# Kernel optimization log

Measured on AMD Instinct MI355X. Metric: run time of the kernel, lower is better.

Reference implementation:

```python
import jax, jax.numpy as jnp
import numpy as np

SIGMA = 2.0
INF = 1.0e6
M, N, H, K, C_IN, C_OUT = 50000, 100000, 32, 15, 64, 64
RADIUS = 2.5


def setup_inputs() -> dict:
    key = jax.random.key(0)
    k1, k2, k3, k4, k5, k6 = jax.random.split(key, 6)
    q_points = jax.random.normal(k1, (M, 3), dtype=jnp.float32)
    s_points = jax.random.normal(k2, (N, 3), dtype=jnp.float32)
    s_feats = jax.random.normal(k3, (N, C_IN), dtype=jnp.float32)
    # index N refers to the padding point (placed at INF)
    neighbor_indices = jax.random.randint(k4, (M, H), 0, N + 1, dtype=jnp.int64)
    weights = jax.random.normal(k5, (K, C_IN, C_OUT), dtype=jnp.float32) * 0.05
    # kernel points inside sphere of RADIUS (stand-in for load_kernels buffer)
    kp = jax.random.normal(k6, (K, 3), dtype=jnp.float32)
    kp = kp / jnp.linalg.norm(kp, axis=1, keepdims=True) * RADIUS * 0.7
    kernel_points = kp.at[0].set(0.0)  # fixed='center'
    return {
        "q_points": q_points,
        "s_points": s_points,
        "s_feats": s_feats,
        "neighbor_indices": neighbor_indices,
        "weights": weights,
        "kernel_points": kernel_points,
    }


def reference(q_points, s_points, s_feats, neighbor_indices, weights, kernel_points):
    # pad support points with an 'infinity' shadow point at index N
    padded_pts = jnp.concatenate([s_points, jnp.full((1, 3), INF, s_points.dtype)], axis=0)
    neighbors = padded_pts[neighbor_indices]                    # (M, H, 3)
    rel = neighbors - q_points[:, None, :]                      # (M, H, 3)
    diff = rel[:, :, None, :] - kernel_points[None, None]       # (M, H, K, 3)
    sq_dist = jnp.sum(diff * diff, axis=-1)                     # (M, H, K)
    nbr_w = jnp.clip(1.0 - jnp.sqrt(sq_dist) / SIGMA, 0.0)      # (M, H, K)

    padded_feats = jnp.concatenate([s_feats, jnp.zeros((1, s_feats.shape[1]), s_feats.dtype)], axis=0)
    nbr_feats = padded_feats[neighbor_indices]                  # (M, H, C_in)

    weighted = jnp.einsum('mhk,mhc->mkc', nbr_w, nbr_feats)     # (M, K, C_in)
    out = jnp.einsum('mkc,kcd->md', weighted, weights)          # (M, C_out)

    # normalize by count of real (non-padding / nonzero-sum) neighbors
    nbr_sum = jnp.sum(nbr_feats, axis=-1)                       # (M, H)
    nbr_num = jnp.sum(nbr_sum > 0.0, axis=-1)                   # (M,)
    nbr_num = jnp.maximum(nbr_num, 1)
    return out / nbr_num[:, None].astype(out.dtype)
```

## Files before the change

### kernel.cpp

```cpp
#include <hip/hip_runtime.h>
#include <hip/hip_bf16.h>

#define MPTS 50000
#define NPTS 100000
#define KK 15
#define TM 16
#define NTILES (MPTS / TM)
#define PGRID 512
#define WTP 1028
#define STP 36
#define STPH 20

typedef __attribute__((ext_vector_type(8))) short short8;
typedef __attribute__((ext_vector_type(4))) short short4v;
typedef __attribute__((ext_vector_type(4))) float floatx4;

static __device__ __forceinline__ unsigned short f2bf(float f) {
    __hip_bfloat16 h = __float2bfloat16(f);
    return *reinterpret_cast<unsigned short*>(&h);
}

static __device__ __forceinline__ short8 lds_load8(const unsigned short* p) {
    const short4v a = *(const short4v*)p;
    const short4v b = *(const short4v*)(p + 4);
    short8 r;
    r[0] = a[0]; r[1] = a[1]; r[2] = a[2]; r[3] = a[3];
    r[4] = b[0]; r[5] = b[1]; r[6] = b[2]; r[7] = b[3];
    return r;
}

static __device__ __forceinline__ unsigned cvtb(unsigned char u) {
    return (unsigned)f2bf((float)(int)(signed char)u);
}

static __device__ __forceinline__ void lds_barrier() {
    asm volatile("s_waitcnt lgkmcnt(0)" ::: "memory");
    __builtin_amdgcn_s_barrier();
    __builtin_amdgcn_sched_barrier(0);
}

__global__ void prep_all(const float* __restrict__ sf, const float* __restrict__ w,
                         const float* __restrict__ kpts, const float* __restrict__ spt,
                         unsigned char* __restrict__ sfb8, float4* __restrict__ spts4,
                         unsigned short* __restrict__ wbf2, float4* __restrict__ kpp) {
    const int b = blockIdx.x, t = threadIdx.x;
    if (b < 782) {
        const int tt = b * 256 + t;
        const int row = tt >> 1, p = tt & 1;
        if (row < NPTS) {
            const float* base = sf + (size_t)row * 64 + p * 4;
            float4 x[8];
            x[0] = *(const float4*)base;
            float4 r = x[0];
            float am = fmaxf(fmaxf(fabsf(x[0].x), fabsf(x[0].y)),
                             fmaxf(fabsf(x[0].z), fabsf(x[0].w)));
#pragma unroll
            for (int i = 1; i < 8; i++) {
                x[i] = *(const float4*)(base + i * 8);
                r.x += x[i].x; r.y += x[i].y; r.z += x[i].z; r.w += x[i].w;
                am = fmaxf(am, fmaxf(fmaxf(fabsf(x[i].x), fabsf(x[i].y)),
                                     fmaxf(fabsf(x[i].z), fabsf(x[i].w))));
            }
            float sp = (r.x + r.y) + (r.z + r.w);
            sp += __shfl_xor(sp, 1);
            am = fmaxf(am, __shfl_xor(am, 1));
            const float inv = am > 0.0f ? 127.0f / am : 0.0f;
#pragma unroll
            for (int i = 0; i < 8; i++) {
                uchar4 o;
                o.x = (unsigned char)(int)rintf(x[i].x * inv);
                o.y = (unsigned char)(int)rintf(x[i].y * inv);
                o.z = (unsigned char)(int)rintf(x[i].z * inv);
                o.w = (unsigned char)(int)rintf(x[i].w * inv);
                *(uchar4*)&sfb8[(size_t)row * 64 + i * 8 + p * 4] = o;
            }
            if (p == 0) {
                const float sc = am * (1.0f / 127.0f);
                spts4[row] = make_float4(spt[row * 3 + 0], spt[row * 3 + 1],
                                         spt[row * 3 + 2], sp > 0.0f ? sc : -sc);
            }
        }
    } else if (b < 814) {
        const int e = (b - 782) * 256 + t;
        const int lane = e & 63, s = (e >> 6) & 31, wq = e >> 11;
        const int d = wq * 16 + (lane & 15);
        const int lqp = lane >> 4;
        unsigned short o8[8];
#pragma unroll
        for (int j = 0; j < 8; j++) {
            const int kc = s * 32 + lqp * 8 + j;
            const int c = kc >> 4, k = kc & 15;
            o8[j] = (k < KK) ? f2bf(w[k * 4096 + c * 64 + d]) : (unsigned short)0;
        }
#pragma unroll
        for (int j = 0; j < 8; j++) wbf2[(size_t)e * 8 + j] = o8[j];
    } else {
        if (t < 16) *(uchar4*)&sfb8[(size_t)NPTS * 64 + t * 4] = make_uchar4(0, 0, 0, 0);
        else if (t == 16) spts4[NPTS] = make_float4(1.0e6f, 1.0e6f, 1.0e6f, -1.0f);
        else if (t >= 32 && t < 32 + KK) {
            const int k = t - 32;
            const float kx = kpts[k * 3 + 0], ky = kpts[k * 3 + 1], kz = kpts[k * 3 + 2];
            kpp[k] = make_float4(-2.f * kx, -2.f * ky, -2.f * kz, kx * kx + ky * ky + kz * kz);
        }
    }
}

__global__ __launch_bounds__(512, 2) void kpconv_fused(
    const float* __restrict__ q_points,
    const float4* __restrict__ spts4,
    const unsigned char* __restrict__ sfb8,
    const int*   __restrict__ nbr,
    const unsigned short* __restrict__ wbf2,
    const float4* __restrict__ kpp,
    float* __restrict__ out)
{
    const int t    = threadIdx.x;
    const int lane = t & 63;
    const int wv   = t >> 6;
    const int l15  = lane & 15;
    const int lq   = lane >> 4;

    __shared__ __align__(16) unsigned short stage[8][64 * STPH];
    __shared__ unsigned short wtw[TM * WTP];
    __shared__ float inv_lds[TM];
    __shared__ __align__(16) float scratch[1024];

    const int mw = 2 * wv + (lane >> 5);
    const int h  = lane & 31;
    const int c4 = l15 * 4;

    const int q  = wv & 3;
    const int kh = wv >> 2;
    const unsigned short* const ap = &wtw[l15 * WTP + kh * 512 + lq * 8];
    const unsigned short* const bp = wbf2 + ((size_t)((q * 32 + kh * 16) * 64) + lane) * 8;

    unsigned short* const st = stage[wv];
    const int swzh = (l15 >> 3) << 2;
    const short8 zero8 = {0, 0, 0, 0, 0, 0, 0, 0};

    uchar4 g[2][8];
    float4 sp4;
    float qx, qy, qz;

    auto PREFETCH = [&](const int m0n) {
        const int idxp = nbr[(size_t)(m0n + mw) * 32 + h];
#pragma unroll
        for (int mi = 0; mi < 2; mi++) {
            const int m = 2 * wv + mi;
#pragma unroll
            for (int g2 = 0; g2 < 4; g2++) {
                const int r0 = g2 * 8 + lq * 2;
                const int2 ip = *(const int2*)&nbr[(size_t)(m0n + m) * 32 + r0];
                const int i0 = min(ip.x, NPTS);
                const int i1 = min(ip.y, NPTS);
                g[mi][2 * g2]     = *(const uchar4*)&sfb8[(size_t)i0 * 64 + c4];
                g[mi][2 * g2 + 1] = *(const uchar4*)&sfb8[(size_t)i1 * 64 + c4];
            }
        }
        sp4 = spts4[min(idxp, NPTS)];
        qx = q_points[(m0n + mw) * 3 + 0];
        qy = q_points[(m0n + mw) * 3 + 1];
        qz = q_points[(m0n + mw) * 3 + 2];
    };

    PREFETCH(blockIdx.x * TM);

    for (int tile = blockIdx.x; tile < NTILES; tile += PGRID) {
        const int m0 = tile * TM;

        {
            const float rx = sp4.x - qx;
            const float ry = sp4.y - qy;
            const float rz = sp4.z - qz;
            const float r2 = rx * rx + ry * ry + rz * rz;
            const float ss = fabsf(sp4.w);
            unsigned short* wrow = &wtw[mw * WTP];
#pragma unroll
            for (int k = 0; k < KK; k++) {
                const float4 kp = kpp[k];
                float d2 = kp.w;
                d2 = fmaf(rx, kp.x, d2);
                d2 = fmaf(ry, kp.y, d2);
                d2 = fmaf(rz, kp.z, d2);
                d2 = fmaxf(r2 + d2, 0.0f);
                const float wv_ = fmaxf(fmaf(-0.5f, __builtin_amdgcn_sqrtf(d2), 1.0f), 0.0f);
                wrow[k * STP + h] = f2bf(wv_ * ss);
            }
            wrow[15 * STP + h] = 0;

            const unsigned long long bal = __ballot(sp4.w > 0.0f);
            if (h == 0) {
                const int cnt = __popc((unsigned)(bal >> ((lane >> 5) * 32)));
                inv_lds[mw] = 1.0f / (float)(cnt < 1 ? 1 : cnt);
            }
        }

#pragma unroll
        for (int mi = 0; mi < 2; mi++) {
            const int m = 2 * wv + mi;
            const short8 afull = lds_load8(&wtw[m * WTP + l15 * STP + lq * 8]);
            floatx4 d[4];
#pragma unroll
            for (int ct = 0; ct < 4; ct++) d[ct] = (floatx4){0.f, 0.f, 0.f, 0.f};
#pragma unroll
            for (int r = 0; r < 2; r++) {
#pragma unroll
                for (int g2h = 0; g2h < 2; g2h++) {
                    const int g2 = 2 * r + g2h;
                    const int so = (((g2h * 4 + lq) ^ swzh)) * 2;
                    const uchar4 a = g[mi][2 * g2];
                    const uchar4 b = g[mi][2 * g2 + 1];
                    *(unsigned*)&st[(c4 + 0) * STPH + so] = cvtb(a.x) | (cvtb(b.x) << 16);
                    *(unsigned*)&st[(c4 + 1) * STPH + so] = cvtb(a.y) | (cvtb(b.y) << 16);
                    *(unsigned*)&st[(c4 + 2) * STPH + so] = cvtb(a.z) | (cvtb(b.z) << 16);
                    *(unsigned*)&st[(c4 + 3) * STPH + so] = cvtb(a.w) | (cvtb(b.w) << 16);
                }
                const short8 ar = ((lq >> 1) == r) ? afull : zero8;
#pragma unroll
                for (int ct = 0; ct < 4; ct++) {
                    const short8 bfrag =
                        lds_load8(&st[(ct * 16 + l15) * STPH + (((lq & 1) ^ (ct >> 1)) * 8)]);
                    d[ct] = __builtin_amdgcn_mfma_f32_16x16x32_bf16(ar, bfrag, d[ct], 0, 0, 0);
                }
            }
#pragma unroll
            for (int ct = 0; ct < 4; ct++) {
                ushort4 pk;
                pk.x = f2bf(d[ct][0]); pk.y = f2bf(d[ct][1]);
                pk.z = f2bf(d[ct][2]); pk.w = f2bf(d[ct][3]);
                *(ushort4*)&wtw[m * WTP + (ct * 16 + l15) * 16 + lq * 4] = pk;
            }
        }

        const int nxt = tile + PGRID;
        if (nxt < NTILES) PREFETCH(nxt * TM);

        lds_barrier();

        {
            float inv4[4];
            if (kh == 0) {
#pragma unroll
                for (int r = 0; r < 4; r++) inv4[r] = inv_lds[lq * 4 + r];
            }
            floatx4 acc = {0.f, 0.f, 0.f, 0.f};
#pragma unroll 8
            for (int s = 0; s < 16; s++) {
                const short8 a = lds_load8(ap + s * 32);
                const short8 b = *(const short8*)(bp + s * 512);
                acc = __builtin_amdgcn_mfma_f32_16x16x32_bf16(a, b, acc, 0, 0, 0);
            }
            if (kh == 1) {
                *(floatx4*)&scratch[q * 256 + l15 * 16 + lq * 4] = acc;
            }

            lds_barrier();

            if (kh == 0) {
                const floatx4 p = *(const floatx4*)&scratch[q * 256 + l15 * 16 + lq * 4];
                const int d = q * 16 + l15;
#pragma unroll
                for (int r = 0; r < 4; r++) {
                    const int m = lq * 4 + r;
                    out[(size_t)(m0 + m) * 64 + d] = (acc[r] + p[r]) * inv4[r];
                }
            }
        }
    }
}

extern "C" void kernel_launch(void* const* d_in, const int* in_sizes, int n_in,
                              void* d_out, int out_size, void* d_ws, size_t ws_size,
                              hipStream_t stream) {
    const float* q_points = (const float*)d_in[0];
    const float* s_points = (const float*)d_in[1];
    const float* s_feats  = (const float*)d_in[2];
    const int*   nbr      = (const int*)d_in[3];
    const float* weights  = (const float*)d_in[4];
    const float* kpts     = (const float*)d_in[5];
    float* out = (float*)d_out;

    char* ws = (char*)d_ws;
    unsigned short* wbf2 = (unsigned short*)ws;
    float4* spts4 = (float4*)(ws + 131072);
    float4* kpp = (float4*)(ws + 1731088);
    unsigned char* sfb8 = (unsigned char*)(ws + 1731584);

    prep_all<<<815, 256, 0, stream>>>(s_feats, weights, kpts, s_points,
                                      sfb8, spts4, wbf2, kpp);
    kpconv_fused<<<PGRID, 512, 0, stream>>>(q_points, spts4, sfb8, nbr,
                                            wbf2, kpp, out);
}
```

Baseline: 142.1 us.

## Replace persistent grid with one-shot blocks processing two tiles each

Drops the persistent loop over 512 blocks in favour of a grid of ceil(M/32) blocks, each handling two 16-point tiles. All gathers for both tiles are issued up front to expose memory-level parallelism. The scratch buffer is aliased onto the stage buffer to cut LDS so three blocks can fit per CU, and launch bounds are raised to match. In exchange, each block pays its own launch and prologue cost, register pressure rises from holding two tiles of gathered data, and extra barriers are needed to make the LDS aliasing safe.

```diff
diff --git a/kernel.cpp b/kernel.cpp
--- a/kernel.cpp
+++ b/kernel.cpp
@@ -5,8 +5,7 @@
 #define NPTS 100000
 #define KK 15
 #define TM 16
-#define NTILES (MPTS / TM)
-#define PGRID 512
+#define GRID ((MPTS + 31) / 32)
 #define WTP 1028
 #define STP 36
 #define STPH 20
@@ -105,7 +104,7 @@
     }
 }
 
-__global__ __launch_bounds__(512, 2) void kpconv_fused(
+__global__ __launch_bounds__(512, 3) void kpconv_fused(
     const float* __restrict__ q_points,
     const float4* __restrict__ spts4,
     const unsigned char* __restrict__ sfb8,
@@ -123,7 +122,6 @@
     __shared__ __align__(16) unsigned short stage[8][64 * STPH];
     __shared__ unsigned short wtw[TM * WTP];
     __shared__ float inv_lds[TM];
-    __shared__ __align__(16) float scratch[1024];
 
     const int mw = 2 * wv + (lane >> 5);
     const int h  = lane & 31;
@@ -133,68 +131,80 @@
     const int kh = wv >> 2;
     const unsigned short* const ap = &wtw[l15 * WTP + kh * 512 + lq * 8];
     const unsigned short* const bp = wbf2 + ((size_t)((q * 32 + kh * 16) * 64) + lane) * 8;
+    float* const scratch = (float*)&stage[0][0];
 
     unsigned short* const st = stage[wv];
     const int swzh = (l15 >> 3) << 2;
     const short8 zero8 = {0, 0, 0, 0, 0, 0, 0, 0};
 
-    uchar4 g[2][8];
-    float4 sp4;
-    float qx, qy, qz;
-
-    auto PREFETCH = [&](const int m0n) {
-        const int idxp = nbr[(size_t)(m0n + mw) * 32 + h];
-#pragma unroll
-        for (int mi = 0; mi < 2; mi++) {
-            const int m = 2 * wv + mi;
-#pragma unroll
-            for (int g2 = 0; g2 < 4; g2++) {
-                const int r0 = g2 * 8 + lq * 2;
-                const int2 ip = *(const int2*)&nbr[(size_t)(m0n + m) * 32 + r0];
-                const int i0 = min(ip.x, NPTS);
-                const int i1 = min(ip.y, NPTS);
-                g[mi][2 * g2]     = *(const uchar4*)&sfb8[(size_t)i0 * 64 + c4];
-                g[mi][2 * g2 + 1] = *(const uchar4*)&sfb8[(size_t)i1 * 64 + c4];
-            }
-        }
-        sp4 = spts4[min(idxp, NPTS)];
-        qx = q_points[(m0n + mw) * 3 + 0];
-        qy = q_points[(m0n + mw) * 3 + 1];
-        qz = q_points[(m0n + mw) * 3 + 2];
+    const int m0a = blockIdx.x * 32;
+    const int m0b = m0a + 16;
+
+    const int ia = nbr[(size_t)(m0a + mw) * 32 + h];
+    const float4 sp4a = spts4[min(ia, NPTS)];
+    uchar4 ga[2][8];
+#pragma unroll
+    for (int mi = 0; mi < 2; mi++) {
+        const int m = 2 * wv + mi;
+#pragma unroll
+        for (int g2 = 0; g2 < 4; g2++) {
+            const int r0 = g2 * 8 + lq * 2;
+            const int2 ip = *(const int2*)&nbr[(size_t)(m0a + m) * 32 + r0];
+            ga[mi][2 * g2]     = *(const uchar4*)&sfb8[(size_t)min(ip.x, NPTS) * 64 + c4];
+            ga[mi][2 * g2 + 1] = *(const uchar4*)&sfb8[(size_t)min(ip.y, NPTS) * 64 + c4];
+        }
+    }
+    const float qax = q_points[(m0a + mw) * 3 + 0];
+    const float qay = q_points[(m0a + mw) * 3 + 1];
+    const float qaz = q_points[(m0a + mw) * 3 + 2];
+
+    const int mrb = min(m0b + mw, MPTS - 1);
+    const int ib = nbr[(size_t)mrb * 32 + h];
+    const float4 sp4b = spts4[min(ib, NPTS)];
+    uchar4 gb[2][8];
+#pragma unroll
+    for (int mi = 0; mi < 2; mi++) {
+        const int m = min(m0b + 2 * wv + mi, MPTS - 1);
+#pragma unroll
+        for (int g2 = 0; g2 < 4; g2++) {
+            const int r0 = g2 * 8 + lq * 2;
+            const int2 ip = *(const int2*)&nbr[(size_t)m * 32 + r0];
+            gb[mi][2 * g2]     = *(const uchar4*)&sfb8[(size_t)min(ip.x, NPTS) * 64 + c4];
+            gb[mi][2 * g2 + 1] = *(const uchar4*)&sfb8[(size_t)min(ip.y, NPTS) * 64 + c4];
+        }
+    }
+    const float qbx = q_points[mrb * 3 + 0];
+    const float qby = q_points[mrb * 3 + 1];
+    const float qbz = q_points[mrb * 3 + 2];
+
+    auto WEIGHTS = [&](const float4 sp4, const float qx, const float qy, const float qz) {
+        const float rx = sp4.x - qx;
+        const float ry = sp4.y - qy;
+        const float rz = sp4.z - qz;
+        const float r2 = rx * rx + ry * ry + rz * rz;
+        const float ss = fabsf(sp4.w);
+        unsigned short* wrow = &wtw[mw * WTP];
+#pragma unroll
+        for (int k = 0; k < KK; k++) {
+            const float4 kp = kpp[k];
+            float d2 = kp.w;
+            d2 = fmaf(rx, kp.x, d2);
+            d2 = fmaf(ry, kp.y, d2);
+            d2 = fmaf(rz, kp.z, d2);
+            d2 = fmaxf(r2 + d2, 0.0f);
+            const float wv_ = fmaxf(fmaf(-0.5f, __builtin_amdgcn_sqrtf(d2), 1.0f), 0.0f);
+            wrow[k * STP + h] = f2bf(wv_ * ss);
+        }
+        wrow[15 * STP + h] = 0;
+
+        const unsigned long long bal = __ballot(sp4.w > 0.0f);
+        if (h == 0) {
+            const int cnt = __popc((unsigned)(bal >> ((lane >> 5) * 32)));
+            inv_lds[mw] = 1.0f / (float)(cnt < 1 ? 1 : cnt);
+        }
     };
 
-    PREFETCH(blockIdx.x * TM);
-
-    for (int tile = blockIdx.x; tile < NTILES; tile += PGRID) {
-        const int m0 = tile * TM;
-
-        {
-            const float rx = sp4.x - qx;
-            const float ry = sp4.y - qy;
-            const float rz = sp4.z - qz;
-            const float r2 = rx * rx + ry * ry + rz * rz;
-            const float ss = fabsf(sp4.w);
-            unsigned short* wrow = &wtw[mw * WTP];
-#pragma unroll
-            for (int k = 0; k < KK; k++) {
-                const float4 kp = kpp[k];
-                float d2 = kp.w;
-                d2 = fmaf(rx, kp.x, d2);
-                d2 = fmaf(ry, kp.y, d2);
-                d2 = fmaf(rz, kp.z, d2);
-                d2 = fmaxf(r2 + d2, 0.0f);
-                const float wv_ = fmaxf(fmaf(-0.5f, __builtin_amdgcn_sqrtf(d2), 1.0f), 0.0f);
-                wrow[k * STP + h] = f2bf(wv_ * ss);
-            }
-            wrow[15 * STP + h] = 0;
-
-            const unsigned long long bal = __ballot(sp4.w > 0.0f);
-            if (h == 0) {
-                const int cnt = __popc((unsigned)(bal >> ((lane >> 5) * 32)));
-                inv_lds[mw] = 1.0f / (float)(cnt < 1 ? 1 : cnt);
-            }
-        }
-
+    auto PHASEB = [&](const uchar4 (&g)[2][8]) {
 #pragma unroll
         for (int mi = 0; mi < 2; mi++) {
             const int m = 2 * wv + mi;
@@ -231,42 +241,47 @@
                 *(ushort4*)&wtw[m * WTP + (ct * 16 + l15) * 16 + lq * 4] = pk;
             }
         }
-
-        const int nxt = tile + PGRID;
-        if (nxt < NTILES) PREFETCH(nxt * TM);
-
-        lds_barrier();
-
-        {
-            float inv4[4];
-            if (kh == 0) {
-#pragma unroll
-                for (int r = 0; r < 4; r++) inv4[r] = inv_lds[lq * 4 + r];
-            }
-            floatx4 acc = {0.f, 0.f, 0.f, 0.f};
+    };
+
+    auto PHASEC = [&](const int m0, const bool store_ok) {
+        float inv4[4];
+        if (kh == 0) {
+#pragma unroll
+            for (int r = 0; r < 4; r++) inv4[r] = inv_lds[lq * 4 + r];
+        }
+        floatx4 acc = {0.f, 0.f, 0.f, 0.f};
 #pragma unroll 8
-            for (int s = 0; s < 16; s++) {
-                const short8 a = lds_load8(ap + s * 32);
-                const short8 b = *(const short8*)(bp + s * 512);
-                acc = __builtin_amdgcn_mfma_f32_16x16x32_bf16(a, b, acc, 0, 0, 0);
-            }
-            if (kh == 1) {
-                *(floatx4*)&scratch[q * 256 + l15 * 16 + lq * 4] = acc;
-            }
-
-            lds_barrier();
-
-            if (kh == 0) {
-                const floatx4 p = *(const floatx4*)&scratch[q * 256 + l15 * 16 + lq * 4];
-                const int d = q * 16 + l15;
-#pragma unroll
-                for (int r = 0; r < 4; r++) {
-                    const int m = lq * 4 + r;
-                    out[(size_t)(m0 + m) * 64 + d] = (acc[r] + p[r]) * inv4[r];
-                }
-            }
-        }
-    }
+        for (int s = 0; s < 16; s++) {
+            const short8 a = lds_load8(ap + s * 32);
+            const short8 b = *(const short8*)(bp + s * 512);
+            acc = __builtin_amdgcn_mfma_f32_16x16x32_bf16(a, b, acc, 0, 0, 0);
+        }
+        if (kh == 1) {
+            *(floatx4*)&scratch[q * 256 + l15 * 16 + lq * 4] = acc;
+        }
+        __syncthreads();
+        if (kh == 0 && store_ok) {
+            const floatx4 p = *(const floatx4*)&scratch[q * 256 + l15 * 16 + lq * 4];
+            const int d = q * 16 + l15;
+#pragma unroll
+            for (int r = 0; r < 4; r++) {
+                const int m = m0 + lq * 4 + r;
+                if (m < MPTS)
+                    out[(size_t)m * 64 + d] = (acc[r] + p[r]) * inv4[r];
+            }
+        }
+    };
+
+    WEIGHTS(sp4a, qax, qay, qaz);
+    PHASEB(ga);
+    lds_barrier();
+    PHASEC(m0a, true);
+
+    WEIGHTS(sp4b, qbx, qby, qbz);
+    __syncthreads();
+    PHASEB(gb);
+    __syncthreads();
+    PHASEC(m0b, true);
 }
 
 extern "C" void kernel_launch(void* const* d_in, const int* in_sizes, int n_in,
@@ -288,6 +303,6 @@
 
     prep_all<<<815, 256, 0, stream>>>(s_feats, weights, kpts, s_points,
                                       sfb8, spts4, wbf2, kpp);
-    kpconv_fused<<<PGRID, 512, 0, stream>>>(q_points, spts4, sfb8, nbr,
-                                            wbf2, kpp, out);
-}
+    kpconv_fused<<<GRID, 512, 0, stream>>>(q_points, spts4, sfb8, nbr,
+                                           wbf2, kpp, out);
+}
```

Result: slower. 145.5 us (+2.4%).
